# Optimization experiments

Hardware: AMD Instinct MI355X
Metric: run time of the kernel (lower is better)

The kernel has to match this reference:

```python
import jax, jax.numpy as jnp
import numpy as np

N, D_IN = 65536, 512
X_DIMS = [512, 2048, 2048, 512]
Y_DIMS = [512, 1024, 512]
T = 2            # n_treatments
OUT_DIM = 1


def setup_inputs() -> dict:
    key = jax.random.key(0)
    ks = iter(jax.random.split(key, 32))
    s = 0.02
    inp = {
        "x": jax.random.normal(next(ks), (N, D_IN), dtype=jnp.float32),
        "treatment": jax.random.randint(next(ks), (N,), 0, T, dtype=jnp.int64),
        # shared trunk MLP (Linear+ReLU after EVERY linear, per original code)
        "Wx0": jax.random.normal(next(ks), (X_DIMS[0], X_DIMS[1]), jnp.float32) * s,
        "bx0": jnp.zeros((X_DIMS[1],), jnp.float32),
        "Wx1": jax.random.normal(next(ks), (X_DIMS[1], X_DIMS[2]), jnp.float32) * s,
        "bx1": jnp.zeros((X_DIMS[2],), jnp.float32),
        "Wx2": jax.random.normal(next(ks), (X_DIMS[2], X_DIMS[3]), jnp.float32) * s,
        "bx2": jnp.zeros((X_DIMS[3],), jnp.float32),
        # per-treatment expert MLPs, stacked on leading T axis
        "Wy0": jax.random.normal(next(ks), (T, Y_DIMS[0], Y_DIMS[1]), jnp.float32) * s,
        "by0": jnp.zeros((T, Y_DIMS[1]), jnp.float32),
        "Wy1": jax.random.normal(next(ks), (T, Y_DIMS[1], Y_DIMS[2]), jnp.float32) * s,
        "by1": jnp.zeros((T, Y_DIMS[2]), jnp.float32),
        # per-treatment output heads
        "Wo": jax.random.normal(next(ks), (T, Y_DIMS[2], OUT_DIM), jnp.float32) * s,
        "bo": jnp.zeros((T, OUT_DIM), jnp.float32),
        # propensity head
        "Wt": jax.random.normal(next(ks), (X_DIMS[3], 1), jnp.float32) * s,
        "bt": jnp.zeros((1,), jnp.float32),
    }
    return inp


def reference(x, treatment, Wx0, bx0, Wx1, bx1, Wx2, bx2,
              Wy0, by0, Wy1, by1, Wo, bo, Wt, bt):
    # shared trunk: ReLU follows every Linear (original MLP applies ReLU after
    # the last layer too, because `i < len(dims)-1` is always true in the loop)
    h = jax.nn.relu(x @ Wx0 + bx0)
    h = jax.nn.relu(h @ Wx1 + bx1)
    x_emb = jax.nn.relu(h @ Wx2 + bx2)            # [N, 512]

    # per-treatment experts computed densely, then gathered by treatment id.
    # This is the dense-equivalent of SplitStreams -> MLP -> GatherStreams:
    # GatherStreams sorts by original row index, so row n of the output is the
    # treatment-`t[n]` head applied to x_emb[n].
    g = jax.nn.relu(jnp.einsum('nd,tdh->nth', x_emb, Wy0) + by0)   # [N,T,1024]
    g = jax.nn.relu(jnp.einsum('nth,thk->ntk', g, Wy1) + by1)      # [N,T,512]
    y_all = jnp.einsum('ntk,tko->nto', g, Wo) + bo                 # [N,T,1]

    t_idx = treatment.astype(jnp.int32).reshape(-1)
    y = jnp.take_along_axis(y_all, t_idx[:, None, None], axis=1)[:, 0, :]  # [N,1]

    # softmax over a size-1 axis -> all ones, but kept faithful to the source
    t_out = jax.nn.softmax(x_emb @ Wt + bt, axis=1)                # [N,1]
    return y, x_emb, t_out
```

## Files before the change

kernel.cpp:

```cpp
#include <hip/hip_runtime.h>
#include <hip/hip_bf16.h>
#include <cstdint>

#define NROWS 65536
#define TTREAT 2

typedef __bf16 bf16x8 __attribute__((ext_vector_type(8)));
typedef float f32x4 __attribute__((ext_vector_type(4)));
typedef unsigned short u16;
typedef u16 u16x8 __attribute__((ext_vector_type(8)));

#define GLOBAL_AS __attribute__((address_space(1)))
#define LDS_AS __attribute__((address_space(3)))

__device__ __forceinline__ int swz_col(int col, int row) {
    return (col & ~63) | (((((col >> 3) & 7) ^ (row & 7)) << 3)) | (col & 7);
}

__device__ __forceinline__ u16 f32_to_bf16_bits(float f) {
    union { float f; uint32_t u; } v; v.f = f;
    uint32_t u = v.u;
    return (u16)((u + 0x7FFFu + ((u >> 16) & 1u)) >> 16);
}

__global__ void cvt_f32_bf16(const float4* __restrict__ src, u16x8* __restrict__ dst, int n8) {
    int i = blockIdx.x * blockDim.x + threadIdx.x;
    if (i >= n8) return;
    float4 a = src[2 * i], b = src[2 * i + 1];
    u16x8 r;
    r[0] = f32_to_bf16_bits(a.x); r[1] = f32_to_bf16_bits(a.y);
    r[2] = f32_to_bf16_bits(a.z); r[3] = f32_to_bf16_bits(a.w);
    r[4] = f32_to_bf16_bits(b.x); r[5] = f32_to_bf16_bits(b.y);
    r[6] = f32_to_bf16_bits(b.z); r[7] = f32_to_bf16_bits(b.w);
    int row = i >> 6;
    int j = (i & ~7) | ((i ^ row) & 7);
    dst[j] = r;
}

__global__ void transpose_w(const float* __restrict__ src, u16* __restrict__ dst, int K, int M) {
    __shared__ float tile[32][33];
    size_t boff = (size_t)blockIdx.z * K * M;
    src += boff; dst += boff;
    int m0 = blockIdx.x * 32, k0 = blockIdx.y * 32;
    int tx = threadIdx.x, ty = threadIdx.y;
#pragma unroll
    for (int i = 0; i < 32; i += 8)
        tile[ty + i][tx] = src[(size_t)(k0 + ty + i) * M + m0 + tx];
    __syncthreads();
#pragma unroll
    for (int i = 0; i < 32; i += 8) {
        int row = m0 + ty + i, col = k0 + tx;
        dst[(size_t)row * K + swz_col(col, row)] = f32_to_bf16_bits(tile[tx][ty + i]);
    }
}

__global__ void zero_cnt(int* cnt) {
    if (threadIdx.x < TTREAT) cnt[threadIdx.x] = 0;
}

__global__ void partition_rows(const int* __restrict__ treat, int* __restrict__ idx, int* __restrict__ cnt) {
    __shared__ int waveCnt1[4];
    __shared__ int blockBase[2];
    const int tid = threadIdx.x;
    const int i = blockIdx.x * 256 + tid;
    const int wave = tid >> 6, lane = tid & 63;
    const int t = treat[i];
    const unsigned long long m1 = __ballot(t == 1);
    const int n1 = __popcll(m1);
    if (lane == 0) waveCnt1[wave] = n1;
    __syncthreads();
    const int w0 = waveCnt1[0], w1 = waveCnt1[1], w2 = waveCnt1[2], w3 = waveCnt1[3];
    const int tot1 = w0 + w1 + w2 + w3;
    if (tid == 0) blockBase[0] = atomicAdd(&cnt[0], 256 - tot1);
    else if (tid == 64) blockBase[1] = atomicAdd(&cnt[1], tot1);
    __syncthreads();
    int waveOff1 = 0;
    if (wave > 0) waveOff1 += w0;
    if (wave > 1) waveOff1 += w1;
    if (wave > 2) waveOff1 += w2;
    const int below1 = (int)__popcll(m1 & ((1ull << lane) - 1ull));
    int pos;
    if (t == 1) pos = blockBase[1] + waveOff1 + below1;
    else        pos = blockBase[0] + (wave * 64 - waveOff1) + (lane - below1);
    idx[t * NROWS + pos] = i;
}

__global__ void init_outputs(const int* __restrict__ treat, const float* __restrict__ bo,
                             float* __restrict__ y, float* __restrict__ t_out) {
    int i = blockIdx.x * 256 + threadIdx.x;
    if (i < NROWS) { y[i] = bo[treat[i]]; t_out[i] = 1.0f; }
}

template <bool GATHER, bool WRITE_F32, bool FUSE_HEAD>
__global__ void gemm_bias_relu(const u16* __restrict__ A, const u16* __restrict__ Bt,
                               const float* __restrict__ bias,
                               u16* __restrict__ C, float* __restrict__ C32,
                               const int* __restrict__ idx, const int* __restrict__ cntp,
                               int nrows, int chunkStart, int maxRows, int K, int M,
                               const float* __restrict__ Wo, float* __restrict__ y) {
    int rows = (cntp ? *cntp : nrows) - chunkStart;
    if (rows > maxRows) rows = maxRows;

    const unsigned gx  = gridDim.x;
    const unsigned nwg = gx * gridDim.y;
    const unsigned lin = blockIdx.y * gx + blockIdx.x;
    const unsigned q = nwg >> 3, r = nwg & 7;
    const unsigned xcd = lin & 7, ii = lin >> 3;
    const unsigned wg = (xcd < r ? xcd * (q + 1) : r * (q + 1) + (xcd - r) * q) + ii;

    int rowBase = (int)(wg / gx) * 128;
    if (rows <= 0 || rowBase >= rows) return;
    int colBase = (int)(wg % gx) * 128;

    __shared__ __align__(16) u16 As[128 * 64];
    __shared__ __align__(16) u16 Bs[128 * 64];

    const int tid = threadIdx.x;
    const int wave = tid >> 6, lane = tid & 63;
    const int quad = lane >> 4, l16 = lane & 15;
    const int wm = wave >> 1, wn = wave & 1;

    const int r0 = tid >> 3;
    const int kc = (tid & 7) * 8;

    size_t a_off[4], b_off[4];
#pragma unroll
    for (int it = 0; it < 4; ++it) {
        int r_ = rowBase + r0 + it * 32;
        if (GATHER) {
            int rc = r_ < rows ? r_ : (rows - 1);
            int g = idx[rc];
            int kcg = ((((tid & 7) ^ (r_ & 7) ^ (g & 7)) & 7) * 8);
            a_off[it] = (size_t)g * K + kcg;
        } else {
            a_off[it] = (size_t)r_ * K + kc;
        }
        int c = colBase + r0 + it * 32;
        b_off[it] = (size_t)c * K + kc;
    }

    f32x4 acc[4][4] = {};

    for (int k0 = 0; k0 < K; k0 += 64) {
        __syncthreads();
#pragma unroll
        for (int it = 0; it < 4; ++it) {
            __builtin_amdgcn_global_load_lds(
                (const GLOBAL_AS void*)(A + a_off[it] + k0),
                (LDS_AS void*)(&As[(it * 256 + wave * 64) * 8]), 16, 0, 0);
            __builtin_amdgcn_global_load_lds(
                (const GLOBAL_AS void*)(Bt + b_off[it] + k0),
                (LDS_AS void*)(&Bs[(it * 256 + wave * 64) * 8]), 16, 0, 0);
        }
        __syncthreads();
#pragma unroll
        for (int kk = 0; kk < 2; ++kk) {
            bf16x8 aF[4], bF[4];
            const int csw = ((kk * 4 + quad) ^ (l16 & 7)) * 8;
#pragma unroll
            for (int mi = 0; mi < 4; ++mi)
                aF[mi] = *(const bf16x8*)&As[(wm * 64 + mi * 16 + l16) * 64 + csw];
#pragma unroll
            for (int ni = 0; ni < 4; ++ni)
                bF[ni] = *(const bf16x8*)&Bs[(wn * 64 + ni * 16 + l16) * 64 + csw];
#pragma unroll
            for (int mi = 0; mi < 4; ++mi)
#pragma unroll
                for (int ni = 0; ni < 4; ++ni)
                    acc[mi][ni] = __builtin_amdgcn_mfma_f32_16x16x32_bf16(
                        aF[mi], bF[ni], acc[mi][ni], 0, 0, 0);
        }
    }

    float bv[4];
#pragma unroll
    for (int ni = 0; ni < 4; ++ni) bv[ni] = bias[colBase + wn * 64 + ni * 16 + l16];

    if (FUSE_HEAD) {
        float wv[4];
#pragma unroll
        for (int ni = 0; ni < 4; ++ni) wv[ni] = Wo[colBase + wn * 64 + ni * 16 + l16];
        float hs[4][4];
#pragma unroll
        for (int mi = 0; mi < 4; ++mi)
#pragma unroll
            for (int r_ = 0; r_ < 4; ++r_) {
                float s = 0.f;
#pragma unroll
                for (int ni = 0; ni < 4; ++ni) {
                    float v = acc[mi][ni][r_] + bv[ni];
                    v = v > 0.f ? v : 0.f;
                    s += v * wv[ni];
                }
                hs[mi][r_] = s;
            }
#pragma unroll
        for (int mi = 0; mi < 4; ++mi)
#pragma unroll
            for (int r_ = 0; r_ < 4; ++r_) {
                float s = hs[mi][r_];
                s += __shfl_down(s, 8, 16);
                s += __shfl_down(s, 4, 16);
                s += __shfl_down(s, 2, 16);
                s += __shfl_down(s, 1, 16);
                if (l16 == 0) {
                    int row = rowBase + wm * 64 + mi * 16 + quad * 4 + r_;
                    if (row < rows) atomicAdd(&y[idx[row]], s);
                }
            }
    } else {
#pragma unroll
        for (int mi = 0; mi < 4; ++mi) {
            int rloc = rowBase + wm * 64 + mi * 16 + quad * 4;
#pragma unroll
            for (int ni = 0; ni < 4; ++ni) {
                int col = colBase + wn * 64 + ni * 16 + l16;
#pragma unroll
                for (int r_ = 0; r_ < 4; ++r_) {
                    int row = rloc + r_;
                    if (row < rows) {
                        float v = acc[mi][ni][r_] + bv[ni];
                        v = v > 0.f ? v : 0.f;
                        C[(size_t)row * M + swz_col(col, row)] = f32_to_bf16_bits(v);
                        if (WRITE_F32) C32[(size_t)row * M + col] = v;
                    }
                }
            }
        }
    }
}

extern "C" void kernel_launch(void* const* d_in, const int* in_sizes, int n_in,
                              void* d_out, int out_size, void* d_ws, size_t ws_size,
                              hipStream_t stream) {
    const float* x   = (const float*)d_in[0];
    const int* treat = (const int*)d_in[1];
    const float* Wx0 = (const float*)d_in[2];
    const float* bx0 = (const float*)d_in[3];
    const float* Wx1 = (const float*)d_in[4];
    const float* bx1 = (const float*)d_in[5];
    const float* Wx2 = (const float*)d_in[6];
    const float* bx2 = (const float*)d_in[7];
    const float* Wy0 = (const float*)d_in[8];
    const float* by0 = (const float*)d_in[9];
    const float* Wy1 = (const float*)d_in[10];
    const float* by1 = (const float*)d_in[11];
    const float* Wo  = (const float*)d_in[12];
    const float* bo  = (const float*)d_in[13];

    float* out_y  = (float*)d_out;
    float* out_xe = out_y + NROWS;
    float* out_t  = out_xe + (size_t)NROWS * 512;

    const size_t FIXED = ((size_t)(2048 * 512 + 2048 * 2048 + 512 * 2048
                          + TTREAT * 1024 * 512 + TTREAT * 512 * 1024
                          + (size_t)NROWS * 512) * 2)
                          + (size_t)TTREAT * NROWS * 4 + (1 << 20);
    int R = 512;
    const int cands[8] = {65536, 32768, 16384, 8192, 4096, 2048, 1024, 512};
    for (int ci = 0; ci < 8; ++ci) {
        if (FIXED + (size_t)cands[ci] * 11264 <= ws_size) { R = cands[ci]; break; }
    }
    const int NCHUNK = NROWS / R;

    size_t off = 0;
    auto carve = [&](size_t bytes) {
        void* p = (char*)d_ws + off;
        off += (bytes + 255) & ~(size_t)255;
        return p;
    };
    u16* Wx0t = (u16*)carve((size_t)2048 * 512 * 2);
    u16* Wx1t = (u16*)carve((size_t)2048 * 2048 * 2);
    u16* Wx2t = (u16*)carve((size_t)512 * 2048 * 2);
    u16* Wy0t = (u16*)carve((size_t)TTREAT * 1024 * 512 * 2);
    u16* Wy1t = (u16*)carve((size_t)TTREAT * 512 * 1024 * 2);
    u16* xe   = (u16*)carve((size_t)NROWS * 512 * 2);
    int* idx  = (int*)carve((size_t)TTREAT * NROWS * 4);
    int* cnt  = (int*)carve(256);
    u16* xbc  = (u16*)carve((size_t)R * 512 * 2);
    u16* h1c  = (u16*)carve((size_t)R * 2048 * 2);
    u16* h2c  = (u16*)carve((size_t)R * 2048 * 2);
    u16* g1c  = (u16*)carve((size_t)R * 1024 * 2);

    dim3 tb32(32, 8);

    transpose_w<<<dim3(2048 / 32, 512 / 32, 1), tb32, 0, stream>>>(Wx0, Wx0t, 512, 2048);
    transpose_w<<<dim3(2048 / 32, 2048 / 32, 1), tb32, 0, stream>>>(Wx1, Wx1t, 2048, 2048);
    transpose_w<<<dim3(512 / 32, 2048 / 32, 1), tb32, 0, stream>>>(Wx2, Wx2t, 2048, 512);
    transpose_w<<<dim3(1024 / 32, 512 / 32, TTREAT), tb32, 0, stream>>>(Wy0, Wy0t, 512, 1024);
    transpose_w<<<dim3(512 / 32, 1024 / 32, TTREAT), tb32, 0, stream>>>(Wy1, Wy1t, 1024, 512);

    zero_cnt<<<1, 64, 0, stream>>>(cnt);
    partition_rows<<<NROWS / 256, 256, 0, stream>>>(treat, idx, cnt);

    init_outputs<<<NROWS / 256, 256, 0, stream>>>(treat, bo, out_y, out_t);

    const int gy = R / 128;

    for (int c = 0; c < NCHUNK; ++c) {
        int cS = c * R;
        cvt_f32_bf16<<<(R * 512 / 8 + 255) / 256, 256, 0, stream>>>(
            (const float4*)(x + (size_t)cS * 512), (u16x8*)xbc, R * 512 / 8);
        gemm_bias_relu<false, false, false><<<dim3(2048 / 128, gy), 256, 0, stream>>>(
            xbc, Wx0t, bx0, h1c, nullptr, nullptr, nullptr, NROWS, cS, R, 512, 2048,
            nullptr, nullptr);
        gemm_bias_relu<false, false, false><<<dim3(2048 / 128, gy), 256, 0, stream>>>(
            h1c, Wx1t, bx1, h2c, nullptr, nullptr, nullptr, NROWS, cS, R, 2048, 2048,
            nullptr, nullptr);
        gemm_bias_relu<false, true, false><<<dim3(512 / 128, gy), 256, 0, stream>>>(
            h2c, Wx2t, bx2, xe + (size_t)cS * 512, out_xe + (size_t)cS * 512,
            nullptr, nullptr, NROWS, cS, R, 2048, 512, nullptr, nullptr);
    }

    for (int t = 0; t < TTREAT; ++t) {
        const int* idx_t = idx + (size_t)t * NROWS;
        for (int c = 0; c < NCHUNK; ++c) {
            int cS = c * R;
            gemm_bias_relu<true, false, false><<<dim3(1024 / 128, gy), 256, 0, stream>>>(
                xe, Wy0t + (size_t)t * 1024 * 512, by0 + (size_t)t * 1024,
                g1c, nullptr, idx_t + cS, cnt + t, NROWS, cS, R, 512, 1024,
                nullptr, nullptr);
            gemm_bias_relu<false, false, true><<<dim3(512 / 128, gy), 256, 0, stream>>>(
                g1c, Wy1t + (size_t)t * 512 * 1024, by1 + (size_t)t * 512,
                nullptr, nullptr, idx_t + cS, cnt + t, NROWS, cS, R, 1024, 512,
                Wo + (size_t)t * 512, out_y);
        }
    }
}
```

Before: 1.417 ms.

## Double-buffer LDS tiles in GEMM to overlap global loads with MFMA

Splits the A and B shared-memory tiles into two buffers. The loads for the next K-slice are issued into the idle buffer before the MFMA work on the current one, and the loop now has one barrier per iteration instead of two. This aims to hide global-to-LDS latency behind compute. In exchange, LDS use per block doubles (64KB), which may lower occupancy. Correctness also depends on the barrier making the async global_load_lds writes complete before the next iteration reads them.

```diff
diff --git a/kernel.cpp b/kernel.cpp
--- a/kernel.cpp
+++ b/kernel.cpp
@@ -112,8 +112,8 @@
     if (rows <= 0 || rowBase >= rows) return;
     int colBase = (int)(wg % gx) * 128;
 
-    __shared__ __align__(16) u16 As[128 * 64];
-    __shared__ __align__(16) u16 Bs[128 * 64];
+    __shared__ __align__(16) u16 As[2][128 * 64];
+    __shared__ __align__(16) u16 Bs[2][128 * 64];
 
     const int tid = threadIdx.x;
     const int wave = tid >> 6, lane = tid & 63;
@@ -139,30 +139,38 @@
         b_off[it] = (size_t)c * K + kc;
     }
 
+#define STAGE_TILE(buf, k0_)                                                   \
+    do {                                                                       \
+        _Pragma("unroll")                                                      \
+        for (int it = 0; it < 4; ++it) {                                       \
+            __builtin_amdgcn_global_load_lds(                                  \
+                (const GLOBAL_AS void*)(A + a_off[it] + (k0_)),                \
+                (LDS_AS void*)(&As[buf][(it * 256 + wave * 64) * 8]), 16, 0, 0);\
+            __builtin_amdgcn_global_load_lds(                                  \
+                (const GLOBAL_AS void*)(Bt + b_off[it] + (k0_)),               \
+                (LDS_AS void*)(&Bs[buf][(it * 256 + wave * 64) * 8]), 16, 0, 0);\
+        }                                                                      \
+    } while (0)
+
     f32x4 acc[4][4] = {};
-
-    for (int k0 = 0; k0 < K; k0 += 64) {
-        __syncthreads();
-#pragma unroll
-        for (int it = 0; it < 4; ++it) {
-            __builtin_amdgcn_global_load_lds(
-                (const GLOBAL_AS void*)(A + a_off[it] + k0),
-                (LDS_AS void*)(&As[(it * 256 + wave * 64) * 8]), 16, 0, 0);
-            __builtin_amdgcn_global_load_lds(
-                (const GLOBAL_AS void*)(Bt + b_off[it] + k0),
-                (LDS_AS void*)(&Bs[(it * 256 + wave * 64) * 8]), 16, 0, 0);
-        }
-        __syncthreads();
+    const int NS = K >> 6;
+
+    STAGE_TILE(0, 0);
+    __syncthreads();
+
+    for (int s = 0; s < NS; ++s) {
+        const int cb = s & 1;
+        if (s + 1 < NS) STAGE_TILE(cb ^ 1, (s + 1) << 6);
 #pragma unroll
         for (int kk = 0; kk < 2; ++kk) {
             bf16x8 aF[4], bF[4];
             const int csw = ((kk * 4 + quad) ^ (l16 & 7)) * 8;
 #pragma unroll
             for (int mi = 0; mi < 4; ++mi)
-                aF[mi] = *(const bf16x8*)&As[(wm * 64 + mi * 16 + l16) * 64 + csw];
+                aF[mi] = *(const bf16x8*)&As[cb][(wm * 64 + mi * 16 + l16) * 64 + csw];
 #pragma unroll
             for (int ni = 0; ni < 4; ++ni)
-                bF[ni] = *(const bf16x8*)&Bs[(wn * 64 + ni * 16 + l16) * 64 + csw];
+                bF[ni] = *(const bf16x8*)&Bs[cb][(wn * 64 + ni * 16 + l16) * 64 + csw];
 #pragma unroll
             for (int mi = 0; mi < 4; ++mi)
 #pragma unroll
@@ -170,7 +178,9 @@
                     acc[mi][ni] = __builtin_amdgcn_mfma_f32_16x16x32_bf16(
                         aF[mi], bF[ni], acc[mi][ni], 0, 0, 0);
         }
-    }
+        __syncthreads();
+    }
+#undef STAGE_TILE
 
     float bv[4];
 #pragma unroll
```

Measured after the change: 1.782 ms. 25.8% more time.
